# Kernel tuning notes

Measured on AMD Instinct MI355X. Metric: run time of the kernel, lower is better.

## Reference

```python
import jax, jax.numpy as jnp
import numpy as np

B, N, D, K = 64, 512, 256, 1024
LIMIT = float(np.sqrt(K))   # default initialize_limit = num_embeddings ** 0.5
BN_EPS = 1e-5               # torch BatchNorm1d default eps


def setup_inputs() -> dict:
    key = jax.random.key(0)
    k1, k2, k3 = jax.random.split(key, 3)
    x = jax.random.normal(k1, (B, N, D), jnp.float32)
    atom_mask = jax.random.randint(k2, (B, N), 0, 2, jnp.int32)
    e_i_ts = jax.random.uniform(k3, (D, K), jnp.float32, -LIMIT, LIMIT)
    return {
        "x": x,
        "atom_mask": atom_mask,
        "e_i_ts": e_i_ts,
        "bn_gamma": jnp.ones((D,), jnp.float32),
        "bn_beta": jnp.zeros((D,), jnp.float32),
    }


def reference(x, atom_mask, e_i_ts, bn_gamma, bn_beta):
    flat = x.reshape(-1, D)                          # [BN, D]
    m = atom_mask.reshape(-1).astype(flat.dtype)     # [BN], 1 = valid atom
    n_valid = jnp.maximum(m.sum(), 1.0)

    # BatchNorm1d (training mode) over valid atoms only (torch applies BN to
    # the gathered rows). Biased variance, as in torch's normalization.
    mu = (m[:, None] * flat).sum(0) / n_valid
    var = (m[:, None] * (flat - mu) ** 2).sum(0) / n_valid
    xb = (flat - mu) * jax.lax.rsqrt(var + BN_EPS) * bn_gamma + bn_beta

    # squared-distance to codebook + argmin + gather
    d = (xb ** 2).sum(1, keepdims=True) - 2.0 * (xb @ e_i_ts) + (e_i_ts ** 2).sum(0, keepdims=True)  # [BN, K]
    idx = jnp.argmin(d, axis=1)                      # [BN]
    q = e_i_ts.T[idx]                                # [BN, D] quantized (valid-row semantics)

    # scatter back into padded tensor (padded rows -> 0), straight-through
    q_pad = (m[:, None] * q).reshape(x.shape)
    quantized_x = x + jax.lax.stop_gradient(q_pad - x)

    sg = jax.lax.stop_gradient
    dictionary_loss = (m[:, None] * (sg(xb) - q) ** 2).sum() / (n_valid * D)
    commitment_loss = (m[:, None] * (xb - sg(q)) ** 2).sum() / (n_valid * D)

    # perplexity over valid atoms
    counts = jnp.zeros((K,), flat.dtype).at[idx].add(m)
    avg_probs = counts / n_valid
    perplexity = jnp.exp(-jnp.sum(avg_probs * jnp.log(avg_probs + 1e-10)))

    idx_out = jnp.where(m > 0, idx, -1)[:, None]     # [BN, 1]; -1 marks padded rows
    return quantized_x, dictionary_loss, commitment_loss, idx_out, perplexity
```

## Files before the change

### kernel.cpp

```cpp
#include <hip/hip_runtime.h>
#include <math.h>

#define BN   32768
#define DIM  256
#define KC   1024
#define BN_EPS 1e-5f

#define QX_SIZE   (BN * DIM)
#define LOSS0_OFF (QX_SIZE)
#define LOSS1_OFF (QX_SIZE + 1)
#define IDX_OFF   (QX_SIZE + 2)
#define PERP_OFF  (QX_SIZE + 2 + BN)

#define PART_V 0
#define PART_I (NSLICE * BN)

#define WS_SUM    0
#define WS_SUMSQ  256
#define WS_COUNT  512
#define WS_LOSS   513
#define WS_COUNTS 1024
#define WS_CNORM  3072
#define WS_PK     8192
#define WS_ETX    (8192 + 262144)
#define WS_MINKEY (8192 + 262144 + 262144)
#define WS_ET_LEG 8192

#define NSLICE 8
#define SLICEK (KC / NSLICE)
#define NGRP   (SLICEK / 64)

typedef short bf16x8  __attribute__((ext_vector_type(8)));
typedef float f32x4   __attribute__((ext_vector_type(4)));
typedef float fvec4   __attribute__((ext_vector_type(4)));
typedef int   int4v   __attribute__((ext_vector_type(4)));
typedef unsigned long long u64;

static __device__ inline unsigned short f2bf(float f) {
    unsigned int u = __float_as_uint(f);
    return (unsigned short)((u + 0x7FFFu + ((u >> 16) & 1u)) >> 16);
}
static __device__ inline fvec4 nt_ld4(const void* p) {
    return __builtin_nontemporal_load((const fvec4*)p);
}
static __device__ inline void nt_st(float* p, float v) {
    __builtin_nontemporal_store(v, p);
}
static __device__ inline unsigned enc_f32(float f) {
    unsigned u = __float_as_uint(f);
    return (u & 0x80000000u) ? ~u : (u | 0x80000000u);
}

__global__ __launch_bounds__(256) void k_pre(const float* __restrict__ x,
                                             const int* __restrict__ mask,
                                             const float* __restrict__ e,
                                             float* __restrict__ ws,
                                             int use_et, int use_pk, int et_off) {
    int t = threadIdx.x;
    int b = blockIdx.x;
    if (b >= 260) {
        if (!use_et && !use_pk) return;
        int b2 = b - 260;
        int d0 = (b2 >> 4) * 64;
        int k0 = (b2 & 15) * 64;
        __shared__ float tile[64][65];
        int c = t & 63;
        int rq = t >> 6;
        #pragma unroll
        for (int p = 0; p < 16; ++p) {
            int dd = p * 4 + rq;
            tile[dd][c] = e[(size_t)(d0 + dd) * KC + k0 + c];
        }
        __syncthreads();
        if (use_et) {
            #pragma unroll
            for (int p = 0; p < 16; ++p) {
                int kk = p * 4 + rq;
                nt_st(&ws[et_off + (size_t)(k0 + kk) * DIM + d0 + c],
                      tile[c][kk]);
            }
        }
        if (use_pk) {
            char* pk = (char*)(ws + WS_PK);
            int lane2 = t & 63;
            int fgrp = t >> 6;
            int quad2 = lane2 >> 4, col2 = lane2 & 15;
            int G = b2 & 15;
            #pragma unroll
            for (int p = 0; p < 4; ++p) {
                int fi = fgrp * 4 + p;
                int kcl = fi >> 3;
                int nt = (fi >> 1) & 3;
                int h = fi & 1;
                int kcg = (b2 >> 4) * 2 + kcl;
                bf16x8 ov;
                #pragma unroll
                for (int j = 0; j < 8; ++j) {
                    float v = tile[kcl * 32 + quad2 * 8 + j][nt * 16 + col2];
                    unsigned u = __float_as_uint(v);
                    if (h == 0) {
                        ov[j] = (short)(u >> 16);
                    } else {
                        float lf = v - __uint_as_float(u & 0xffff0000u);
                        ov[j] = (short)(__float_as_uint(lf) >> 16);
                    }
                }
                size_t off = ((size_t)((G * 8 + kcg) * 8 + nt * 2 + h) << 10)
                             + (size_t)lane2 * 16;
                *(bf16x8*)(pk + off) = ov;
            }
        }
        return;
    }
    if (b >= 256) {
        int k = (b - 256) * 256 + t;
        float acc = 0.f;
        #pragma unroll 8
        for (int d = 0; d < DIM; ++d) {
            float v = e[(size_t)d * KC + k];
            acc = fmaf(v, v, acc);
        }
        ws[WS_CNORM + k] = acc;
        return;
    }
    __shared__ float s4[4 * 256];
    __shared__ float q4[4 * 256];
    __shared__ float cntS[4];
    int c4 = t & 63;
    int rsub = t >> 6;
    float s0=0.f,s1=0.f,s2=0.f,s3=0.f, q0=0.f,q1=0.f,q2=0.f,q3=0.f, cnt=0.f;
    int rbase = b * 4 + rsub;
    for (int i = 0; i < 32; ++i) {
        int r = rbase + i * 1024;
        float m = (float)mask[r];
        fvec4 v = nt_ld4(&x[(size_t)r * DIM + c4 * 4]);
        cnt += m;
        float m0 = m*v.x, m1 = m*v.y, m2 = m*v.z, m3 = m*v.w;
        s0 += m0; s1 += m1; s2 += m2; s3 += m3;
        q0 = fmaf(m0, v.x, q0); q1 = fmaf(m1, v.y, q1);
        q2 = fmaf(m2, v.z, q2); q3 = fmaf(m3, v.w, q3);
    }
    int f = c4 * 4;
    s4[rsub * 256 + f + 0] = s0; s4[rsub * 256 + f + 1] = s1;
    s4[rsub * 256 + f + 2] = s2; s4[rsub * 256 + f + 3] = s3;
    q4[rsub * 256 + f + 0] = q0; q4[rsub * 256 + f + 1] = q1;
    q4[rsub * 256 + f + 2] = q2; q4[rsub * 256 + f + 3] = q3;
    if (c4 == 0) cntS[rsub] = cnt;
    __syncthreads();
    float stot = s4[t] + s4[256 + t] + s4[512 + t] + s4[768 + t];
    float qtot = q4[t] + q4[256 + t] + q4[512 + t] + q4[768 + t];
    atomicAdd(&ws[WS_SUM + t], stot);
    atomicAdd(&ws[WS_SUMSQ + t], qtot);
    if (t == 0)
        atomicAdd(&ws[WS_COUNT], cntS[0] + cntS[1] + cntS[2] + cntS[3]);
}


#define CHUNK_COMPUTE(slot, kcc)                                             \
    {                                                                        \
        const char* bufb = &Bs[(slot) * 8192];                               \
        __builtin_amdgcn_s_setprio(1);                                       \
        _Pragma("unroll")                                                    \
        for (int nt = 0; nt < 4; ++nt) {                                     \
            bf16x8 bh = *(const bf16x8*)(bufb + (nt * 2 + 0) * 1024 + lane * 16); \
            bf16x8 bl = *(const bf16x8*)(bufb + (nt * 2 + 1) * 1024 + lane * 16); \
            acc[nt] = __builtin_amdgcn_mfma_f32_16x16x32_bf16(ah[kcc], bh, acc[nt], 0, 0, 0); \
            acc[nt] = __builtin_amdgcn_mfma_f32_16x16x32_bf16(ah[kcc], bl, acc[nt], 0, 0, 0); \
            acc[nt] = __builtin_amdgcn_mfma_f32_16x16x32_bf16(al[kcc], bh, acc[nt], 0, 0, 0); \
        }                                                                    \
        __builtin_amdgcn_s_setprio(0);                                       \
    }

#define SCORE_MERGE(gg)                                                      \
    {                                                                        \
        _Pragma("unroll")                                                    \
        for (int r = 0; r < 4; ++r) {                                        \
            float v = 3.4e38f; int ii = 0;                                   \
            _Pragma("unroll")                                                \
            for (int nt = 0; nt < 4; ++nt) {                                 \
                int kl = (gg) * 64 + nt * 16 + col0;                         \
                float sc = fmaf(-2.f, acc[nt][r], cnS[kl]);                  \
                if (sc < v) { v = sc; ii = kl; }                             \
            }                                                                \
            _Pragma("unroll")                                                \
            for (int m2 = 1; m2 < 16; m2 <<= 1) {                            \
                float v2 = __shfl_xor(v, m2, 64);                            \
                int   i2 = __shfl_xor(ii, m2, 64);                           \
                if (v2 < v || (v2 == v && i2 < ii)) { v = v2; ii = i2; }     \
            }                                                                \
            if (v < bv[r] || (v == bv[r] && ii < bi_[r])) {                  \
                bv[r] = v; bi_[r] = ii;                                      \
            }                                                                \
        }                                                                    \
        _Pragma("unroll")                                                    \
        for (int nt = 0; nt < 4; ++nt)                                       \
            acc[nt] = (f32x4){0.f, 0.f, 0.f, 0.f};                           \
    }

__global__ __launch_bounds__(512, 4) void k_main_mfma(
        const float* __restrict__ x, const int* __restrict__ mask,
        const float* __restrict__ e, const float* __restrict__ gamma,
        const float* __restrict__ beta,
        float* __restrict__ ws, float* __restrict__ out,
        int use_pk, int use_mk) {
    __shared__ __align__(16) char Bs[4 * 8192];
    __shared__ float muS[DIM], scS[DIM], btS[DIM];
    __shared__ float cnS[SLICEK];

    const int tid = threadIdx.x;
    const int rb = blockIdx.x >> 3;
    const int s = blockIdx.x & 7;
    const int row0 = rb * 128;
    const int w = tid >> 6;
    const int lane = tid & 63;
    const int quad = lane >> 4;
    const int col0 = lane & 15;

    if (tid < 256) {
        float cnt = ws[WS_COUNT];
        float nv = fmaxf(cnt, 1.f);
        float mu = ws[WS_SUM + tid] / nv;
        float var = ws[WS_SUMSQ + tid] / nv - mu * mu;
        var = fmaxf(var, 0.f);
        muS[tid] = mu;
        scS[tid] = rsqrtf(var + BN_EPS) * gamma[tid];
        btS[tid] = beta[tid];
    }
    if (tid < SLICEK)
        cnS[tid] = ws[WS_CNORM + s * SLICEK + tid];
    __syncthreads();

    bf16x8 ah[8], al[8];
    {
        const float* xr = x + (size_t)(row0 + w * 16 + col0) * DIM;
        #pragma unroll
        for (int kc = 0; kc < 8; ++kc) {
            int k0 = kc * 32 + quad * 8;
            fvec4 v0 = nt_ld4(xr + k0);
            fvec4 v1 = nt_ld4(xr + k0 + 4);
            float xv[8] = {v0.x, v0.y, v0.z, v0.w, v1.x, v1.y, v1.z, v1.w};
            bf16x8 hv, lv;
            #pragma unroll
            for (int j = 0; j < 8; ++j) {
                float xb = fmaf(xv[j] - muS[k0 + j], scS[k0 + j], btS[k0 + j]);
                unsigned short h = f2bf(xb);
                float hf = __uint_as_float((unsigned)h << 16);
                hv[j] = (short)h;
                lv[j] = (short)f2bf(xb - hf);
            }
            ah[kc] = hv;
            al[kc] = lv;
        }
    }
    asm volatile("s_waitcnt vmcnt(0)" ::: "memory");
    __builtin_amdgcn_sched_barrier(0);

    f32x4 acc[4];
    #pragma unroll
    for (int nt = 0; nt < 4; ++nt)
        acc[nt] = (f32x4){0.f, 0.f, 0.f, 0.f};
    float bv[4] = {3.4e38f, 3.4e38f, 3.4e38f, 3.4e38f};
    int   bi_[4] = {0, 0, 0, 0};

    if (use_pk) {
        const char* pkb = (const char*)(ws + WS_PK)
                          + (size_t)s * (NGRP * 8 * 8192);
        auto stage = [&](int c2, int slot) {
            const char* src = pkb + (size_t)c2 * 8192 + w * 1024 + lane * 16;
            char* dst = &Bs[slot * 8192 + w * 1024];
            __builtin_amdgcn_global_load_lds(
                (const __attribute__((address_space(1))) void*)src,
                (__attribute__((address_space(3))) void*)dst, 16, 0, 0);
        };
        stage(0, 0);
        stage(1, 1);
        for (int g = 0; g < NGRP - 1; ++g) {
            #pragma unroll
            for (int kc = 0; kc < 8; ++kc) {
                stage(g * 8 + kc + 2, (kc + 2) & 3);
                asm volatile("s_waitcnt vmcnt(2)" ::: "memory");
                __builtin_amdgcn_s_barrier();
                __builtin_amdgcn_sched_barrier(0);
                CHUNK_COMPUTE(kc & 3, kc);
            }
            SCORE_MERGE(g);
        }
        {
            #pragma unroll
            for (int kc = 0; kc < 8; ++kc) {
                if (kc < 6) {
                    stage((NGRP - 1) * 8 + kc + 2, (kc + 2) & 3);
                    asm volatile("s_waitcnt vmcnt(2)" ::: "memory");
                } else if (kc == 6) {
                    asm volatile("s_waitcnt vmcnt(1)" ::: "memory");
                } else {
                    asm volatile("s_waitcnt vmcnt(0)" ::: "memory");
                }
                __builtin_amdgcn_s_barrier();
                __builtin_amdgcn_sched_barrier(0);
                CHUNK_COMPUTE(kc & 3, kc);
            }
            SCORE_MERGE(NGRP - 1);
        }
    } else {
        for (int g = 0; g < NGRP; ++g) {
            #pragma unroll
            for (int kc = 0; kc < 8; ++kc) {
                const float* ep = e + (size_t)(kc * 32 + quad * 8) * KC
                                    + s * SLICEK + g * 64 + col0;
                #pragma unroll
                for (int nt = 0; nt < 4; ++nt) {
                    const float* epn = ep + nt * 16;
                    float bvv[8];
                    #pragma unroll
                    for (int j = 0; j < 8; ++j)
                        bvv[j] = epn[(size_t)j * KC];
                    int4v hw, lw;
                    #pragma unroll
                    for (int p = 0; p < 4; ++p) {
                        unsigned u0 = __float_as_uint(bvv[2 * p]);
                        unsigned u1 = __float_as_uint(bvv[2 * p + 1]);
                        hw[p] = (int)__builtin_amdgcn_perm(u1, u0, 0x07060302u);
                        float l0 = bvv[2 * p]     - __uint_as_float(u0 & 0xffff0000u);
                        float l1 = bvv[2 * p + 1] - __uint_as_float(u1 & 0xffff0000u);
                        lw[p] = (int)__builtin_amdgcn_perm(__float_as_uint(l1),
                                                           __float_as_uint(l0),
                                                           0x07060302u);
                    }
                    bf16x8 bh = __builtin_bit_cast(bf16x8, hw);
                    bf16x8 bl = __builtin_bit_cast(bf16x8, lw);
                    acc[nt] = __builtin_amdgcn_mfma_f32_16x16x32_bf16(ah[kc], bh, acc[nt], 0, 0, 0);
                    acc[nt] = __builtin_amdgcn_mfma_f32_16x16x32_bf16(ah[kc], bl, acc[nt], 0, 0, 0);
                    acc[nt] = __builtin_amdgcn_mfma_f32_16x16x32_bf16(al[kc], bh, acc[nt], 0, 0, 0);
                }
            }
            SCORE_MERGE(g);
        }
    }

    if (col0 == 0) {
        if (use_mk) {
            u64* mk = (u64*)(ws + WS_MINKEY);
            #pragma unroll
            for (int r = 0; r < 4; ++r) {
                int rl = w * 16 + quad * 4 + r;
                u64 key = ((u64)enc_f32(bv[r]) << 32)
                          | (unsigned)(s * SLICEK + bi_[r]);
                atomicMin(&mk[row0 + rl], key);
            }
        } else {
            #pragma unroll
            for (int r = 0; r < 4; ++r) {
                int rl = w * 16 + quad * 4 + r;
                out[PART_V + s * BN + row0 + rl] = bv[r];
                out[PART_I + s * BN + row0 + rl] = (float)(s * SLICEK + bi_[r]);
            }
        }
    }
}

__global__ __launch_bounds__(256) void k_merge(const int* __restrict__ mask,
                                               float* __restrict__ ws,
                                               float* __restrict__ out) {
    int row = blockIdx.x * 256 + threadIdx.x;
    float bvv = out[PART_V + row];
    int bii = (int)out[PART_I + row];
    #pragma unroll
    for (int s = 1; s < NSLICE; ++s) {
        float v = out[PART_V + s * BN + row];
        int i = (int)out[PART_I + s * BN + row];
        if (v < bvv || (v == bvv && i < bii)) { bvv = v; bii = i; }
    }
    int m = mask[row];
    out[IDX_OFF + row] = m ? (float)bii : -1.0f;
    if (m) atomicAdd(&ws[WS_COUNTS + bii], 1.0f);
}

__global__ __launch_bounds__(256) void k_epi(
        const float* __restrict__ x, const int* __restrict__ mask,
        const float* __restrict__ e, const float* __restrict__ gamma,
        const float* __restrict__ beta,
        const float* __restrict__ ws, float* __restrict__ out,
        int use_et, int et_off, int use_mk) {
    __shared__ __align__(16) float muS[DIM], scS[DIM], btS[DIM];
    __shared__ int   histC[KC];
    __shared__ float wred[4];
    const int tid = threadIdx.x;
    const int row0 = blockIdx.x * 32;
    const int w = tid >> 6;
    const int lane = tid & 63;
    {
        float cnt = ws[WS_COUNT];
        float nv = fmaxf(cnt, 1.f);
        float mu = ws[WS_SUM + tid] / nv;
        float var = ws[WS_SUMSQ + tid] / nv - mu * mu;
        var = fmaxf(var, 0.f);
        muS[tid] = mu;
        scS[tid] = rsqrtf(var + BN_EPS) * gamma[tid];
        btS[tid] = beta[tid];
    }
    #pragma unroll
    for (int j = 0; j < KC / 256; ++j)
        histC[j * 256 + tid] = 0;
    __syncthreads();

    u64 mykey = 0; int mym = 0;
    if (use_mk && lane < 8) {
        const u64* mk = (const u64*)(ws + WS_MINKEY);
        mykey = mk[row0 + w * 8 + lane];
        mym = mask[row0 + w * 8 + lane];
    }

    const int d0 = lane * 4;
    fvec4 mu4 = *(const fvec4*)&muS[d0];
    fvec4 sc4 = *(const fvec4*)&scS[d0];
    fvec4 bt4 = *(const fvec4*)&btS[d0];
    const float* et = ws + et_off;
    float lacc = 0.f;
    int pidx = -1;
    fvec4 g = (fvec4){0.f, 0.f, 0.f, 0.f};
    #pragma unroll
    for (int rr = 0; rr < 8; ++rr) {
        const int row = row0 + w * 8 + rr;
        int m, idx;
        if (use_mk) {
            u64 k = __shfl(mykey, rr, 64);
            m = __shfl(mym, rr, 64);
            idx = (int)(unsigned)(k & 0xFFFFFFFFull);
            if (lane == 0) {
                out[IDX_OFF + row] = m ? (float)idx : -1.0f;
                if (m) atomicAdd(&histC[idx], 1);
            }
        } else {
            m = mask[row];
            idx = m ? (int)out[IDX_OFF + row] : 0;
        }
        const float fm = (float)m;
        fvec4 xv = nt_ld4(&x[(size_t)row * DIM + d0]);
        if (idx != pidx) {
            if (use_mk || !use_et) {
                g.x = e[(size_t)(d0 + 0) * KC + idx];
                g.y = e[(size_t)(d0 + 1) * KC + idx];
                g.z = e[(size_t)(d0 + 2) * KC + idx];
                g.w = e[(size_t)(d0 + 3) * KC + idx];
            } else {
                g = nt_ld4(&et[(size_t)idx * DIM + d0]);
            }
            pidx = idx;
        }
        fvec4 q;
        float dsum = 0.f;
        #pragma unroll
        for (int i = 0; i < 4; ++i) {
            float xb = fmaf(xv[i] - mu4[i], sc4[i], bt4[i]);
            float diff = xb - g[i];
            dsum = fmaf(diff, diff, dsum);
            q[i] = fm * g[i];
        }
        lacc = fmaf(fm, dsum, lacc);
        __builtin_nontemporal_store(q, (fvec4*)&out[(size_t)row * DIM + d0]);
    }
    #pragma unroll
    for (int off2 = 32; off2 > 0; off2 >>= 1)
        lacc += __shfl_down(lacc, off2, 64);
    if (lane == 0) wred[w] = lacc;
    __syncthreads();
    if (use_mk) {
        #pragma unroll
        for (int j = 0; j < KC / 256; ++j) {
            int c = histC[j * 256 + tid];
            if (c > 0) atomicAdd((float*)&ws[WS_COUNTS + j * 256 + tid],
                                 (float)c);
        }
    }
    if (tid == 0)
        atomicAdd((float*)&ws[WS_LOSS], wred[0] + wred[1] + wred[2] + wred[3]);
}

__global__ __launch_bounds__(256) void k_final(const float* __restrict__ ws,
                                               float* __restrict__ out) {
    int t = threadIdx.x;
    __shared__ float wr[4];
    float nv = fmaxf(ws[WS_COUNT], 1.f);
    float acc = 0.f;
    for (int j = t; j < KC; j += 256) {
        float p = ws[WS_COUNTS + j] / nv;
        acc = fmaf(p, logf(p + 1e-10f), acc);
    }
    #pragma unroll
    for (int off = 32; off > 0; off >>= 1) acc += __shfl_down(acc, off, 64);
    if ((t & 63) == 0) wr[t >> 6] = acc;
    __syncthreads();
    if (t == 0) {
        float ent = wr[0] + wr[1] + wr[2] + wr[3];
        float loss = ws[WS_LOSS] / (nv * (float)DIM);
        out[LOSS0_OFF] = loss;
        out[LOSS1_OFF] = loss;
        out[PERP_OFF] = expf(-ent);
    }
}

extern "C" void kernel_launch(void* const* d_in, const int* in_sizes, int n_in,
                              void* d_out, int out_size, void* d_ws, size_t ws_size,
                              hipStream_t stream) {
    const float* x     = (const float*)d_in[0];
    const int*   amask = (const int*)d_in[1];
    const float* e     = (const float*)d_in[2];
    const float* gamma = (const float*)d_in[3];
    const float* beta  = (const float*)d_in[4];
    float* out = (float*)d_out;
    float* ws  = (float*)d_ws;

    size_t need_mk = (size_t)(WS_MINKEY + 2 * BN) * sizeof(float);
    size_t need_pk = (size_t)(WS_ETX + KC * DIM) * sizeof(float);
    size_t need_et = (size_t)(WS_ET_LEG + KC * DIM) * sizeof(float);
    int use_pk = ws_size >= need_pk;
    int use_mk = use_pk && (ws_size >= need_mk);
    int use_et = use_mk ? 0 : (use_pk ? 1 : (ws_size >= need_et ? 1 : 0));
    int et_off = use_pk ? WS_ETX : WS_ET_LEG;

    (void)hipMemsetAsync(d_ws, 0, 32768, stream);
    if (use_mk)
        (void)hipMemsetAsync((char*)d_ws + (size_t)WS_MINKEY * 4, 0xFF,
                             (size_t)BN * 8, stream);

    k_pre<<<324, 256, 0, stream>>>(x, amask, e, ws, use_et, use_pk, et_off);
    k_main_mfma<<<256 * NSLICE, 512, 0, stream>>>(x, amask, e, gamma, beta, ws,
                                                  out, use_pk, use_mk);
    if (!use_mk)
        k_merge<<<BN / 256, 256, 0, stream>>>(amask, ws, out);
    k_epi<<<BN / 32, 256, 0, stream>>>(x, amask, e, gamma, beta, ws, out,
                                       use_et, et_off, use_mk);
    k_final<<<1, 256, 0, stream>>>(ws, out);
}
```

Baseline: 254.5 us.

## Prepack normalized bf16 A operand once and halve codebook slice count

```diff
diff --git a/kernel.cpp b/kernel.cpp
--- a/kernel.cpp
+++ b/kernel.cpp
@@ -26,7 +26,7 @@
 #define WS_MINKEY (8192 + 262144 + 262144)
 #define WS_ET_LEG 8192
 
-#define NSLICE 8
+#define NSLICE 4
 #define SLICEK (KC / NSLICE)
 #define NGRP   (SLICEK / 64)
 
@@ -153,6 +153,52 @@
     atomicAdd(&ws[WS_SUMSQ + t], qtot);
     if (t == 0)
         atomicAdd(&ws[WS_COUNT], cntS[0] + cntS[1] + cntS[2] + cntS[3]);
+}
+
+__global__ __launch_bounds__(512) void k_packA(
+        const float* __restrict__ x, const float* __restrict__ gamma,
+        const float* __restrict__ beta, const float* __restrict__ ws,
+        float* __restrict__ out) {
+    __shared__ float muS[DIM], scS[DIM], btS[DIM];
+    const int tid = threadIdx.x;
+    const int row0 = blockIdx.x * 128;
+    const int w = tid >> 6;
+    const int lane = tid & 63;
+    const int quad = lane >> 4;
+    const int col0 = lane & 15;
+    if (tid < 256) {
+        float cnt = ws[WS_COUNT];
+        float nv = fmaxf(cnt, 1.f);
+        float mu = ws[WS_SUM + tid] / nv;
+        float var = ws[WS_SUMSQ + tid] / nv - mu * mu;
+        var = fmaxf(var, 0.f);
+        muS[tid] = mu;
+        scS[tid] = rsqrtf(var + BN_EPS) * gamma[tid];
+        btS[tid] = beta[tid];
+    }
+    __syncthreads();
+    const float* xr = x + (size_t)(row0 + w * 16 + col0) * DIM;
+    char* pa = (char*)out + (size_t)(blockIdx.x * 8 + w) * 16384;
+    #pragma unroll
+    for (int kc = 0; kc < 8; ++kc) {
+        int k0 = kc * 32 + quad * 8;
+        fvec4 v0 = nt_ld4(xr + k0);
+        fvec4 v1 = nt_ld4(xr + k0 + 4);
+        float xv[8] = {v0.x, v0.y, v0.z, v0.w, v1.x, v1.y, v1.z, v1.w};
+        bf16x8 hv, lv;
+        #pragma unroll
+        for (int j = 0; j < 8; ++j) {
+            float xb = fmaf(xv[j] - muS[k0 + j], scS[k0 + j], btS[k0 + j]);
+            unsigned short h = f2bf(xb);
+            float hf = __uint_as_float((unsigned)h << 16);
+            hv[j] = (short)h;
+            lv[j] = (short)f2bf(xb - hf);
+        }
+        __builtin_nontemporal_store(hv,
+            (bf16x8*)(pa + (kc * 2 + 0) * 1024 + lane * 16));
+        __builtin_nontemporal_store(lv,
+            (bf16x8*)(pa + (kc * 2 + 1) * 1024 + lane * 16));
+    }
 }
 
 
@@ -202,21 +248,21 @@
         const float* __restrict__ e, const float* __restrict__ gamma,
         const float* __restrict__ beta,
         float* __restrict__ ws, float* __restrict__ out,
-        int use_pk, int use_mk) {
+        int use_pk, int use_mk, int use_pa) {
     __shared__ __align__(16) char Bs[4 * 8192];
     __shared__ float muS[DIM], scS[DIM], btS[DIM];
     __shared__ float cnS[SLICEK];
 
     const int tid = threadIdx.x;
-    const int rb = blockIdx.x >> 3;
-    const int s = blockIdx.x & 7;
+    const int rb = blockIdx.x >> 2;
+    const int s = blockIdx.x & 3;
     const int row0 = rb * 128;
     const int w = tid >> 6;
     const int lane = tid & 63;
     const int quad = lane >> 4;
     const int col0 = lane & 15;
 
-    if (tid < 256) {
+    if (!use_pa && tid < 256) {
         float cnt = ws[WS_COUNT];
         float nv = fmaxf(cnt, 1.f);
         float mu = ws[WS_SUM + tid] / nv;
@@ -231,7 +277,14 @@
     __syncthreads();
 
     bf16x8 ah[8], al[8];
-    {
+    if (use_pa) {
+        const char* pa = (const char*)out + (size_t)(rb * 8 + w) * 16384;
+        #pragma unroll
+        for (int kc = 0; kc < 8; ++kc) {
+            ah[kc] = *(const bf16x8*)(pa + (kc * 2 + 0) * 1024 + lane * 16);
+            al[kc] = *(const bf16x8*)(pa + (kc * 2 + 1) * 1024 + lane * 16);
+        }
+    } else {
         const float* xr = x + (size_t)(row0 + w * 16 + col0) * DIM;
         #pragma unroll
         for (int kc = 0; kc < 8; ++kc) {
@@ -516,6 +569,7 @@
     size_t need_et = (size_t)(WS_ET_LEG + KC * DIM) * sizeof(float);
     int use_pk = ws_size >= need_pk;
     int use_mk = use_pk && (ws_size >= need_mk);
+    int use_pa = use_pk && use_mk;
     int use_et = use_mk ? 0 : (use_pk ? 1 : (ws_size >= need_et ? 1 : 0));
     int et_off = use_pk ? WS_ETX : WS_ET_LEG;
 
@@ -525,8 +579,10 @@
                              (size_t)BN * 8, stream);
 
     k_pre<<<324, 256, 0, stream>>>(x, amask, e, ws, use_et, use_pk, et_off);
+    if (use_pa)
+        k_packA<<<BN / 128, 512, 0, stream>>>(x, gamma, beta, ws, out);
     k_main_mfma<<<256 * NSLICE, 512, 0, stream>>>(x, amask, e, gamma, beta, ws,
-                                                  out, use_pk, use_mk);
+                                                  out, use_pk, use_mk, use_pa);
     if (!use_mk)
         k_merge<<<BN / 256, 256, 0, stream>>>(amask, ws, out);
     k_epi<<<BN / 32, 256, 0, stream>>>(x, amask, e, gamma, beta, ws, out,
```

Measured after the change: 229.5 us. 1.11x faster.
